# Kernel optimization log

Measured on AMD Instinct MI355X. Metric: run time of the kernel, lower is better.

## Reference

```python
import jax, jax.numpy as jnp
import numpy as np

HIDDEN = 1024
HEADS = 16
HEAD = HIDDEN // HEADS


def setup_inputs() -> dict:
    key = jax.random.key(0)
    ks = jax.random.split(key, 10)
    s = 1.0 / np.sqrt(HIDDEN)
    inp = {
        "x": jax.random.normal(ks[0], (2, 2048, HIDDEN), dtype=jnp.float32),
        "Wq": jax.random.uniform(ks[1], (HIDDEN, HIDDEN), jnp.float32, -s, s),
        "bq": jnp.zeros((HIDDEN,), jnp.float32),
        "Wk": jax.random.uniform(ks[2], (HIDDEN, HIDDEN), jnp.float32, -s, s),
        "bk": jnp.zeros((HIDDEN,), jnp.float32),
        "Wv": jax.random.uniform(ks[3], (HIDDEN, HIDDEN), jnp.float32, -s, s),
        "bv": jnp.zeros((HIDDEN,), jnp.float32),
        "Wo": jax.random.uniform(ks[4], (HIDDEN, HIDDEN), jnp.float32, -s, s),
        "bo": jnp.zeros((HIDDEN,), jnp.float32),
        "ln_g": jnp.ones((HIDDEN,), jnp.float32),
        "ln_b": jnp.zeros((HIDDEN,), jnp.float32),
    }
    return inp


def reference(x, Wq, bq, Wk, bk, Wv, bv, Wo, bo, ln_g, ln_b):
    B, S, H = x.shape
    # pre-LN (eps=1e-5 like torch LayerNorm)
    mu = jnp.mean(x, axis=-1, keepdims=True)
    var = jnp.mean(jnp.square(x - mu), axis=-1, keepdims=True)
    xn = (x - mu) * jax.lax.rsqrt(var + 1e-5) * ln_g + ln_b
    # QKV projections (torch Linear: x @ W.T + b) -> [B,S,heads,head]
    q = (xn @ Wq.T + bq).reshape(B, S, HEADS, HEAD)
    k = (xn @ Wk.T + bk).reshape(B, S, HEADS, HEAD)
    v = (xn @ Wv.T + bv).reshape(B, S, HEADS, HEAD)
    # scaled dot-product attention, naive full scores [B,heads,S,S]
    scores = jnp.einsum("bqhd,bkhd->bhqk", q, k) / jnp.sqrt(jnp.float32(HEAD))
    attn = jax.nn.softmax(scores, axis=-1)
    ctx = jnp.einsum("bhqk,bkhd->bqhd", attn, v).reshape(B, S, H)
    out = ctx @ Wo.T + bo
    return x + out  # dropout is identity in eval
```

## Files before the change

kernel.cpp:

```cpp
#include <hip/hip_runtime.h>
#include <hip/hip_bf16.h>
#include <stdint.h>

#define HID 1024
#define SEQ 2048
#define BATCH 2
#define NHEADS 16
#define HEADDIM 64
#define MROWS (BATCH*SEQ)

#define GAS __attribute__((address_space(1)))
#define LAS __attribute__((address_space(3)))

typedef __attribute__((ext_vector_type(8))) __bf16 bf16x8;
typedef __attribute__((ext_vector_type(4))) float f32x4;
typedef __attribute__((ext_vector_type(16))) float f32x16;

__device__ __forceinline__ ushort f2bf(float f) {
  union { float f; uint32_t u; } v; v.f = f;
  return (ushort)((v.u + 0x7FFFu + ((v.u >> 16) & 1u)) >> 16);
}

__device__ __forceinline__ void gl_lds16(const void* g, void* l) {
  __builtin_amdgcn_global_load_lds((const GAS void*)g, (LAS void*)l, 16, 0, 0);
}

__device__ __forceinline__ uint32_t cvtpk(float a, float b) {
  uint32_t r;
  asm("v_cvt_pk_bf16_f32 %0, %1, %2" : "=v"(r) : "v"(a), "v"(b));
  return r;
}

__device__ __forceinline__ void pl32swap(uint32_t& a, uint32_t& b) {
  asm("v_permlane32_swap_b32 %0, %1" : "+v"(a), "+v"(b));
}

__global__ __launch_bounds__(256) void k_cvt(const float* __restrict__ Wq,
                                             const float* __restrict__ Wk,
                                             const float* __restrict__ Wv,
                                             const float* __restrict__ Wo,
                                             ushort* __restrict__ dst) {
  int mat = blockIdx.y;
  const float* src = (mat == 0) ? Wq : (mat == 1) ? Wk : (mat == 2) ? Wv : Wo;
  int off = (blockIdx.x * 256 + threadIdx.x) * 4;
  float4 v = *(const float4*)(src + off);
  ushort4 o;
  o.x = f2bf(v.x); o.y = f2bf(v.y); o.z = f2bf(v.z); o.w = f2bf(v.w);
  *(ushort4*)(dst + (size_t)mat * (HID * HID) + off) = o;
}

__global__ __launch_bounds__(256) void k_ln(const float* __restrict__ x,
                                            const float* __restrict__ g,
                                            const float* __restrict__ b,
                                            ushort* __restrict__ xn) {
  int row = blockIdx.x;
  int t = threadIdx.x;
  const float* xr = x + (size_t)row * HID;
  float4 v = *(const float4*)(xr + t * 4);
  float s = v.x + v.y + v.z + v.w;
  float s2 = v.x * v.x + v.y * v.y + v.z * v.z + v.w * v.w;
  for (int m = 1; m < 64; m <<= 1) { s += __shfl_xor(s, m); s2 += __shfl_xor(s2, m); }
  __shared__ float ws[4], ws2[4];
  int wid = t >> 6;
  if ((t & 63) == 0) { ws[wid] = s; ws2[wid] = s2; }
  __syncthreads();
  s = ws[0] + ws[1] + ws[2] + ws[3];
  s2 = ws2[0] + ws2[1] + ws2[2] + ws2[3];
  float mu = s * (1.0f / HID);
  float var = s2 * (1.0f / HID) - mu * mu;
  float rstd = rsqrtf(var + 1e-5f);
  float4 gg = *(const float4*)(g + t * 4);
  float4 bb = *(const float4*)(b + t * 4);
  ushort4 o;
  o.x = f2bf((v.x - mu) * rstd * gg.x + bb.x);
  o.y = f2bf((v.y - mu) * rstd * gg.y + bb.y);
  o.z = f2bf((v.z - mu) * rstd * gg.z + bb.z);
  o.w = f2bf((v.w - mu) * rstd * gg.w + bb.w);
  *(ushort4*)(xn + (size_t)row * HID + t * 4) = o;
}

__global__ __launch_bounds__(256) void k_qkv(const ushort* __restrict__ xn,
                                             const ushort* __restrict__ wmat,
                                             const float* __restrict__ bq,
                                             const float* __restrict__ bk,
                                             const float* __restrict__ bv,
                                             ushort* __restrict__ qo,
                                             ushort* __restrict__ ko,
                                             ushort* __restrict__ vo) {
  __shared__ ushort As[128 * 32];
  __shared__ ushort Bs[128 * 32];
  int tid = threadIdx.x;
  int lane = tid & 63;
  int wv = tid >> 6;
  int quad = lane >> 4;
  int l16 = lane & 15;
  int m0 = blockIdx.x * 128;
  int ng = blockIdx.y * 128;
  int mat = ng >> 10;
  int nloc = ng & 1023;
  const ushort* wptr = wmat + (size_t)mat * (HID * HID) + (size_t)nloc * HID;
  const float* bias = (mat == 0) ? bq : (mat == 1) ? bk : bv;
  ushort* outp = (mat == 0) ? qo : (mat == 1) ? ko : vo;
  const float scl = (mat == 0) ? 0.18033688011112042f : 1.0f;

  int arow = tid >> 2;
  int acol = (tid & 3) * 8;
  int wm = (wv >> 1) * 64, wn = (wv & 1) * 64;

  f32x4 acc[4][4] = {};
  for (int k0 = 0; k0 < HID; k0 += 32) {
    __syncthreads();
    for (int t = 0; t < 2; t++) {
      gl_lds16(xn + (size_t)(m0 + t * 64 + arow) * HID + k0 + acol,
               As + t * 2048 + wv * 512);
      gl_lds16(wptr + (size_t)(t * 64 + arow) * HID + k0 + acol,
               Bs + t * 2048 + wv * 512);
    }
    __syncthreads();
    bf16x8 af[4], bfr[4];
    for (int i = 0; i < 4; i++)
      af[i] = *(const bf16x8*)&As[(wm + i * 16 + l16) * 32 + quad * 8];
    for (int n = 0; n < 4; n++)
      bfr[n] = *(const bf16x8*)&Bs[(wn + n * 16 + l16) * 32 + quad * 8];
    for (int i = 0; i < 4; i++)
      for (int n = 0; n < 4; n++)
        acc[i][n] = __builtin_amdgcn_mfma_f32_16x16x32_bf16(af[i], bfr[n], acc[i][n], 0, 0, 0);
  }
  float bv4[4];
  for (int n = 0; n < 4; n++) bv4[n] = bias[nloc + wn + n * 16 + l16];
  for (int i = 0; i < 4; i++) {
    int mrow = m0 + wm + i * 16 + quad * 4;
    for (int n = 0; n < 4; n++) {
      int col = nloc + wn + n * 16 + l16;
      int h = col >> 6, d = col & 63;
      for (int r = 0; r < 4; r++) {
        int m = mrow + r;
        int bidx = m >> 11, sidx = m & 2047;
        size_t dst;
        if (mat == 2)
          dst = (((size_t)(bidx * NHEADS + h) * HEADDIM) + d) * SEQ + sidx;
        else
          dst = (((size_t)(bidx * NHEADS + h) * SEQ) + sidx) * HEADDIM + d;
        outp[dst] = f2bf((acc[i][n][r] + bv4[n]) * scl);
      }
    }
  }
}

#define E2(x) __builtin_amdgcn_exp2f(x)

#define SOFTMAX_PF(S0, S1)                                                     \
    union { uint32_t u[4]; bf16x8 v; } pf0, pf1, pf2, pf3;                     \
    {                                                                          \
      uint32_t c0 = cvtpk(E2(S0[0]),  E2(S0[1]));                              \
      uint32_t c1 = cvtpk(E2(S0[2]),  E2(S0[3]));                              \
      uint32_t c2 = cvtpk(E2(S0[4]),  E2(S0[5]));                              \
      uint32_t c3 = cvtpk(E2(S0[6]),  E2(S0[7]));                              \
      uint32_t c4 = cvtpk(E2(S0[8]),  E2(S0[9]));                              \
      uint32_t c5 = cvtpk(E2(S0[10]), E2(S0[11]));                             \
      uint32_t c6 = cvtpk(E2(S0[12]), E2(S0[13]));                             \
      uint32_t c7 = cvtpk(E2(S0[14]), E2(S0[15]));                             \
      pl32swap(c0, c2); pl32swap(c1, c3); pl32swap(c4, c6); pl32swap(c5, c7);  \
      pf0.u[0] = c0; pf0.u[1] = c1; pf0.u[2] = c2; pf0.u[3] = c3;              \
      pf1.u[0] = c4; pf1.u[1] = c5; pf1.u[2] = c6; pf1.u[3] = c7;              \
    }                                                                          \
    {                                                                          \
      uint32_t c0 = cvtpk(E2(S1[0]),  E2(S1[1]));                              \
      uint32_t c1 = cvtpk(E2(S1[2]),  E2(S1[3]));                              \
      uint32_t c2 = cvtpk(E2(S1[4]),  E2(S1[5]));                              \
      uint32_t c3 = cvtpk(E2(S1[6]),  E2(S1[7]));                              \
      uint32_t c4 = cvtpk(E2(S1[8]),  E2(S1[9]));                              \
      uint32_t c5 = cvtpk(E2(S1[10]), E2(S1[11]));                             \
      uint32_t c6 = cvtpk(E2(S1[12]), E2(S1[13]));                             \
      uint32_t c7 = cvtpk(E2(S1[14]), E2(S1[15]));                             \
      pl32swap(c0, c2); pl32swap(c1, c3); pl32swap(c4, c6); pl32swap(c5, c7);  \
      pf2.u[0] = c0; pf2.u[1] = c1; pf2.u[2] = c2; pf2.u[3] = c3;              \
      pf3.u[0] = c4; pf3.u[1] = c5; pf3.u[2] = c6; pf3.u[3] = c7;              \
    }

#define ATTN_BODY(T, SC0, SC1, SP0, SP1, DO_DMA, WAITN)                        \
  do {                                                                         \
    if (DO_DMA) {                                                              \
      size_t ko = (size_t)((T) + 2) * 64 * HEADDIM;                            \
      size_t vo = (size_t)((T) + 2) * 64;                                      \
      gl_lds16(kSrcA + ko, &Ksm[kd][ldsA]);                                    \
      gl_lds16(kSrcB + ko, &Ksm[kd][ldsB]);                                    \
      gl_lds16(vSrcA + vo, &Vsm[vd][ldsA]);                                    \
      gl_lds16(vSrcB + vo, &Vsm[vd][ldsB]);                                    \
    }                                                                          \
    SC0 = (f32x16){}; SC1 = (f32x16){};                                        \
    __builtin_amdgcn_s_setprio(1);                                             \
    _Pragma("unroll")                                                          \
    for (int f = 0; f < 4; f++) {                                              \
      int g = 2 * f + hi;                                                      \
      bf16x8 k0 = *(const bf16x8*)&Ksm[kr][l32 * 64 + ((g ^ rsw) * 8)];        \
      bf16x8 k1 = *(const bf16x8*)&Ksm[kr][(32 + l32) * 64 + ((g ^ rsw) * 8)]; \
      SC0 = __builtin_amdgcn_mfma_f32_32x32x16_bf16(k0, qf[f], SC0, 0, 0, 0);  \
      SC1 = __builtin_amdgcn_mfma_f32_32x32x16_bf16(k1, qf[f], SC1, 0, 0, 0);  \
    }                                                                          \
    __builtin_amdgcn_s_setprio(0);                                             \
    bf16x8 vf[8];                                                              \
    _Pragma("unroll")                                                          \
    for (int kf = 0; kf < 4; kf++) {                                           \
      int g = 2 * kf + hi;                                                     \
      vf[2 * kf]     = *(const bf16x8*)&Vsm[vr][l32 * 64 + ((g ^ rsw) * 8)];   \
      vf[2 * kf + 1] = *(const bf16x8*)&Vsm[vr][(32 + l32) * 64 + ((g ^ rsw) * 8)]; \
    }                                                                          \
    SOFTMAX_PF(SP0, SP1)                                                       \
    __builtin_amdgcn_s_setprio(1);                                             \
    _Pragma("unroll")                                                          \
    for (int kf = 0; kf < 4; kf++) {                                           \
      bf16x8 pv = (kf == 0) ? pf0.v : (kf == 1) ? pf1.v : (kf == 2) ? pf2.v : pf3.v; \
      Oa0 = __builtin_amdgcn_mfma_f32_32x32x16_bf16(pv, vf[2 * kf], Oa0, 0, 0, 0);   \
      Oa1 = __builtin_amdgcn_mfma_f32_32x32x16_bf16(pv, vf[2 * kf + 1], Oa1, 0, 0, 0); \
      Os  = __builtin_amdgcn_mfma_f32_32x32x16_bf16(pv, ones, Os, 0, 0, 0);    \
    }                                                                          \
    __builtin_amdgcn_s_setprio(0);                                             \
    asm volatile("s_waitcnt vmcnt(" #WAITN ")" ::: "memory");                  \
    __builtin_amdgcn_s_barrier();                                              \
    __builtin_amdgcn_sched_barrier(0);                                         \
    kr = (kr == 2) ? 0 : kr + 1;                                               \
    kd = (kd == 2) ? 0 : kd + 1;                                               \
    vr = (vr + 1) & 3;                                                         \
    vd = (vd + 1) & 3;                                                         \
  } while (0)

__global__ __launch_bounds__(256, 2) void k_attn(const ushort* __restrict__ Q,
                                                 const ushort* __restrict__ K,
                                                 const ushort* __restrict__ Vt,
                                                 ushort* __restrict__ ctx) {
  __shared__ ushort Ksm[3][64 * 64];
  __shared__ ushort Vsm[4][64 * 64];
  int tid = threadIdx.x, lane = tid & 63, wv = tid >> 6;
  int l32 = lane & 31, hi = lane >> 5;
  int bh = blockIdx.x;
  int q0 = blockIdx.y * 128;
  const ushort* Qb = Q + ((size_t)bh * SEQ + q0 + wv * 32 + l32) * HEADDIM;
  const ushort* Kb = K + (size_t)bh * SEQ * HEADDIM;
  const ushort* Vb = Vt + (size_t)bh * HEADDIM * SEQ;

  bf16x8 qf[4];
#pragma unroll
  for (int f = 0; f < 4; f++)
    qf[f] = *(const bf16x8*)(Qb + f * 16 + hi * 8);

  bf16x8 ones;
#pragma unroll
  for (int j = 0; j < 8; j++) ones[j] = (__bf16)1.0f;

  int gsl = lane & 7;
  int rowA = wv * 8 + (lane >> 3);
  int rowB = 32 + wv * 8 + (lane >> 3);
  const ushort* kSrcA = Kb + rowA * HEADDIM + ((gsl ^ (rowA & 7)) * 8);
  const ushort* kSrcB = Kb + rowB * HEADDIM + ((gsl ^ (rowB & 7)) * 8);
  const ushort* vSrcA = Vb + (size_t)rowA * SEQ + ((gsl ^ (rowA & 7)) * 8);
  const ushort* vSrcB = Vb + (size_t)rowB * SEQ + ((gsl ^ (rowB & 7)) * 8);
  int ldsA = wv * 512;
  int ldsB = 2048 + wv * 512;

  f32x16 Oa0 = {}, Oa1 = {}, Os = {};
  f32x16 sA0, sA1, sB0, sB1;
  int rsw = (l32 & 7);

  gl_lds16(kSrcA, &Ksm[0][ldsA]);
  gl_lds16(kSrcB, &Ksm[0][ldsB]);
  gl_lds16(vSrcA, &Vsm[0][ldsA]);
  gl_lds16(vSrcB, &Vsm[0][ldsB]);
  gl_lds16(kSrcA + 64 * HEADDIM, &Ksm[1][ldsA]);
  gl_lds16(kSrcB + 64 * HEADDIM, &Ksm[1][ldsB]);
  gl_lds16(vSrcA + 64, &Vsm[1][ldsA]);
  gl_lds16(vSrcB + 64, &Vsm[1][ldsB]);
  asm volatile("s_waitcnt vmcnt(4)" ::: "memory");
  __builtin_amdgcn_s_barrier();
  __builtin_amdgcn_sched_barrier(0);

  {
    gl_lds16(kSrcA + 2 * 64 * HEADDIM, &Ksm[2][ldsA]);
    gl_lds16(kSrcB + 2 * 64 * HEADDIM, &Ksm[2][ldsB]);
    gl_lds16(vSrcA + 2 * 64, &Vsm[2][ldsA]);
    gl_lds16(vSrcB + 2 * 64, &Vsm[2][ldsB]);
    sA0 = (f32x16){}; sA1 = (f32x16){};
    __builtin_amdgcn_s_setprio(1);
#pragma unroll
    for (int f = 0; f < 4; f++) {
      int g = 2 * f + hi;
      bf16x8 k0 = *(const bf16x8*)&Ksm[0][l32 * 64 + ((g ^ rsw) * 8)];
      bf16x8 k1 = *(const bf16x8*)&Ksm[0][(32 + l32) * 64 + ((g ^ rsw) * 8)];
      sA0 = __builtin_amdgcn_mfma_f32_32x32x16_bf16(k0, qf[f], sA0, 0, 0, 0);
      sA1 = __builtin_amdgcn_mfma_f32_32x32x16_bf16(k1, qf[f], sA1, 0, 0, 0);
    }
    __builtin_amdgcn_s_setprio(0);
    asm volatile("s_waitcnt vmcnt(4)" ::: "memory");
    __builtin_amdgcn_s_barrier();
    __builtin_amdgcn_sched_barrier(0);
  }

  int kr = 1, kd = 0, vr = 0, vd = 3;
  for (int t = 1; t < 29; t += 2) {
    ATTN_BODY(t,     sB0, sB1, sA0, sA1, true, 4);
    ATTN_BODY(t + 1, sA0, sA1, sB0, sB1, true, 4);
  }
  ATTN_BODY(29, sB0, sB1, sA0, sA1, true, 4);
  ATTN_BODY(30, sA0, sA1, sB0, sB1, false, 0);

  {
    sB0 = (f32x16){}; sB1 = (f32x16){};
    __builtin_amdgcn_s_setprio(1);
#pragma unroll
    for (int f = 0; f < 4; f++) {
      int g = 2 * f + hi;
      bf16x8 k0 = *(const bf16x8*)&Ksm[kr][l32 * 64 + ((g ^ rsw) * 8)];
      bf16x8 k1 = *(const bf16x8*)&Ksm[kr][(32 + l32) * 64 + ((g ^ rsw) * 8)];
      sB0 = __builtin_amdgcn_mfma_f32_32x32x16_bf16(k0, qf[f], sB0, 0, 0, 0);
      sB1 = __builtin_amdgcn_mfma_f32_32x32x16_bf16(k1, qf[f], sB1, 0, 0, 0);
    }
    __builtin_amdgcn_s_setprio(0);
    bf16x8 vf[8];
#pragma unroll
    for (int kf = 0; kf < 4; kf++) {
      int g = 2 * kf + hi;
      vf[2 * kf]     = *(const bf16x8*)&Vsm[vr][l32 * 64 + ((g ^ rsw) * 8)];
      vf[2 * kf + 1] = *(const bf16x8*)&Vsm[vr][(32 + l32) * 64 + ((g ^ rsw) * 8)];
    }
    SOFTMAX_PF(sA0, sA1)
    __builtin_amdgcn_s_setprio(1);
#pragma unroll
    for (int kf = 0; kf < 4; kf++) {
      bf16x8 pv = (kf == 0) ? pf0.v : (kf == 1) ? pf1.v : (kf == 2) ? pf2.v : pf3.v;
      Oa0 = __builtin_amdgcn_mfma_f32_32x32x16_bf16(pv, vf[2 * kf], Oa0, 0, 0, 0);
      Oa1 = __builtin_amdgcn_mfma_f32_32x32x16_bf16(pv, vf[2 * kf + 1], Oa1, 0, 0, 0);
      Os  = __builtin_amdgcn_mfma_f32_32x32x16_bf16(pv, ones, Os, 0, 0, 0);
    }
    __builtin_amdgcn_s_setprio(0);
    vr = (vr + 1) & 3;
  }

  {
    bf16x8 vf[8];
#pragma unroll
    for (int kf = 0; kf < 4; kf++) {
      int g = 2 * kf + hi;
      vf[2 * kf]     = *(const bf16x8*)&Vsm[vr][l32 * 64 + ((g ^ rsw) * 8)];
      vf[2 * kf + 1] = *(const bf16x8*)&Vsm[vr][(32 + l32) * 64 + ((g ^ rsw) * 8)];
    }
    SOFTMAX_PF(sB0, sB1)
    __builtin_amdgcn_s_setprio(1);
#pragma unroll
    for (int kf = 0; kf < 4; kf++) {
      bf16x8 pv = (kf == 0) ? pf0.v : (kf == 1) ? pf1.v : (kf == 2) ? pf2.v : pf3.v;
      Oa0 = __builtin_amdgcn_mfma_f32_32x32x16_bf16(pv, vf[2 * kf], Oa0, 0, 0, 0);
      Oa1 = __builtin_amdgcn_mfma_f32_32x32x16_bf16(pv, vf[2 * kf + 1], Oa1, 0, 0, 0);
      Os  = __builtin_amdgcn_mfma_f32_32x32x16_bf16(pv, ones, Os, 0, 0, 0);
    }
    __builtin_amdgcn_s_setprio(0);
  }

  int bidx = bh >> 4, h = bh & 15;
#pragma unroll
  for (int r = 0; r < 16; r++) {
    float inv = 1.0f / Os[r];
    int qloc = (r & 3) + 8 * (r >> 2) + 4 * hi;
    int sidx = q0 + wv * 32 + qloc;
    size_t base = ((size_t)(bidx * SEQ) + sidx) * HID + h * HEADDIM;
    ctx[base + l32]      = f2bf(Oa0[r] * inv);
    ctx[base + 32 + l32] = f2bf(Oa1[r] * inv);
  }
}

__global__ __launch_bounds__(256) void k_oproj(const ushort* __restrict__ ctx,
                                               const ushort* __restrict__ wmat,
                                               const float* __restrict__ bo,
                                               const float* __restrict__ x,
                                               float* __restrict__ out) {
  __shared__ ushort As[128 * 32];
  __shared__ ushort Bs[128 * 32];
  int tid = threadIdx.x;
  int lane = tid & 63;
  int wv = tid >> 6;
  int quad = lane >> 4;
  int l16 = lane & 15;
  int m0 = blockIdx.x * 128;
  int n0 = blockIdx.y * 128;
  const ushort* wptr = wmat + (size_t)3 * (HID * HID) + (size_t)n0 * HID;
  int arow = tid >> 2;
  int acol = (tid & 3) * 8;
  int wm = (wv >> 1) * 64, wn = (wv & 1) * 64;

  f32x4 acc[4][4] = {};
  for (int k0 = 0; k0 < HID; k0 += 32) {
    __syncthreads();
    for (int t = 0; t < 2; t++) {
      gl_lds16(ctx + (size_t)(m0 + t * 64 + arow) * HID + k0 + acol,
               As + t * 2048 + wv * 512);
      gl_lds16(wptr + (size_t)(t * 64 + arow) * HID + k0 + acol,
               Bs + t * 2048 + wv * 512);
    }
    __syncthreads();
    bf16x8 af[4], bfr[4];
    for (int i = 0; i < 4; i++)
      af[i] = *(const bf16x8*)&As[(wm + i * 16 + l16) * 32 + quad * 8];
    for (int n = 0; n < 4; n++)
      bfr[n] = *(const bf16x8*)&Bs[(wn + n * 16 + l16) * 32 + quad * 8];
    for (int i = 0; i < 4; i++)
      for (int n = 0; n < 4; n++)
        acc[i][n] = __builtin_amdgcn_mfma_f32_16x16x32_bf16(af[i], bfr[n], acc[i][n], 0, 0, 0);
  }
  float bv4[4];
  for (int n = 0; n < 4; n++) bv4[n] = bo[n0 + wn + n * 16 + l16];
  for (int i = 0; i < 4; i++) {
    int mrow = m0 + wm + i * 16 + quad * 4;
    for (int n = 0; n < 4; n++) {
      int col = n0 + wn + n * 16 + l16;
      for (int r = 0; r < 4; r++) {
        size_t idx = (size_t)(mrow + r) * HID + col;
        out[idx] = acc[i][n][r] + bv4[n] + x[idx];
      }
    }
  }
}

extern "C" void kernel_launch(void* const* d_in, const int* in_sizes, int n_in,
                              void* d_out, int out_size, void* d_ws, size_t ws_size,
                              hipStream_t stream) {
  const float* x    = (const float*)d_in[0];
  const float* Wq   = (const float*)d_in[1];
  const float* bq   = (const float*)d_in[2];
  const float* Wk   = (const float*)d_in[3];
  const float* bk   = (const float*)d_in[4];
  const float* Wv   = (const float*)d_in[5];
  const float* bv   = (const float*)d_in[6];
  const float* Wo   = (const float*)d_in[7];
  const float* bo   = (const float*)d_in[8];
  const float* ln_g = (const float*)d_in[9];
  const float* ln_b = (const float*)d_in[10];
  float* out = (float*)d_out;

  const size_t MB = 1024 * 1024;
  ushort* ws_w = (ushort*)d_ws;
  ushort* xn   = (ushort*)((char*)d_ws + 8 * MB);
  ushort* Qw   = (ushort*)((char*)d_ws + 16 * MB);
  ushort* Kw   = (ushort*)((char*)d_ws + 24 * MB);
  ushort* Vw   = (ushort*)((char*)d_ws + 32 * MB);
  ushort* Cw   = (ushort*)((char*)d_ws + 40 * MB);

  k_cvt<<<dim3(1024, 4), 256, 0, stream>>>(Wq, Wk, Wv, Wo, ws_w);
  k_ln<<<dim3(MROWS), 256, 0, stream>>>(x, ln_g, ln_b, xn);
  k_qkv<<<dim3(32, 24), 256, 0, stream>>>(xn, ws_w, bq, bk, bv, Qw, Kw, Vw);
  k_attn<<<dim3(BATCH * NHEADS, SEQ / 128), 256, 0, stream>>>(Qw, Kw, Vw, Cw);
  k_oproj<<<dim3(32, 8), 256, 0, stream>>>(Cw, ws_w, bo, x, out);
}
```

Measured before the change: 200.4 us.

## Split attention key tiles across wave pairs with LDS cross-wave reduction

Reorganizes the attention kernel so each wave handles 64 query rows and half of each 64-key tile, instead of 32 query rows and the full tile. Each K fragment read from LDS is now reused for two Q fragments, which halves per-wave LDS reads of K and V. The two key-halves' partial outputs and row sums are combined at the end through an LDS reduction in a reused arena. The cost is more accumulator registers per wave, extra barriers, and a final reduction step.

```diff
diff --git a/kernel.cpp b/kernel.cpp
--- a/kernel.cpp
+++ b/kernel.cpp
@@ -148,6 +148,7 @@
 }
 
 #define E2(x) __builtin_amdgcn_exp2f(x)
+#define MFMA(a, b, c) __builtin_amdgcn_mfma_f32_32x32x16_bf16(a, b, c, 0, 0, 0)
 
 #define SOFTMAX_PF(S0, S1)                                                     \
     union { uint32_t u[4]; bf16x8 v; } pf0, pf1, pf2, pf3;                     \
@@ -178,71 +179,72 @@
       pf3.u[0] = c4; pf3.u[1] = c5; pf3.u[2] = c6; pf3.u[3] = c7;              \
     }
 
+#define PV_STEP(VS, SP0, SP1)                                                  \
+    bf16x8 vf00 = *(const bf16x8*)&VSM(VS)[l32 * 64 + (((wk4 + hi) ^ rsw) * 8)];           \
+    bf16x8 vf10 = *(const bf16x8*)&VSM(VS)[l32 * 64 + (((wk4 + 2 + hi) ^ rsw) * 8)];       \
+    bf16x8 vf01 = *(const bf16x8*)&VSM(VS)[(32 + l32) * 64 + (((wk4 + hi) ^ rsw) * 8)];    \
+    bf16x8 vf11 = *(const bf16x8*)&VSM(VS)[(32 + l32) * 64 + (((wk4 + 2 + hi) ^ rsw) * 8)];\
+    SOFTMAX_PF(SP0, SP1)                                                       \
+    __builtin_amdgcn_s_setprio(1);                                             \
+    Oa00 = MFMA(pf0.v, vf00, Oa00); Oa00 = MFMA(pf1.v, vf10, Oa00);            \
+    Oa01 = MFMA(pf0.v, vf01, Oa01); Oa01 = MFMA(pf1.v, vf11, Oa01);            \
+    Oa10 = MFMA(pf2.v, vf00, Oa10); Oa10 = MFMA(pf3.v, vf10, Oa10);            \
+    Oa11 = MFMA(pf2.v, vf01, Oa11); Oa11 = MFMA(pf3.v, vf11, Oa11);            \
+    Os0  = MFMA(pf0.v, ones, Os0);  Os0  = MFMA(pf1.v, ones, Os0);             \
+    Os1  = MFMA(pf2.v, ones, Os1);  Os1  = MFMA(pf3.v, ones, Os1);             \
+    __builtin_amdgcn_s_setprio(0);
+
 #define ATTN_BODY(T, SC0, SC1, SP0, SP1, DO_DMA, WAITN)                        \
   do {                                                                         \
     if (DO_DMA) {                                                              \
       size_t ko = (size_t)((T) + 2) * 64 * HEADDIM;                            \
       size_t vo = (size_t)((T) + 2) * 64;                                      \
-      gl_lds16(kSrcA + ko, &Ksm[kd][ldsA]);                                    \
-      gl_lds16(kSrcB + ko, &Ksm[kd][ldsB]);                                    \
-      gl_lds16(vSrcA + vo, &Vsm[vd][ldsA]);                                    \
-      gl_lds16(vSrcB + vo, &Vsm[vd][ldsB]);                                    \
+      gl_lds16(kSrcA + ko, KSM(kd) + ldsA);                                    \
+      gl_lds16(kSrcB + ko, KSM(kd) + ldsB);                                    \
+      gl_lds16(vSrcA + vo, VSM(vd) + ldsA);                                    \
+      gl_lds16(vSrcB + vo, VSM(vd) + ldsB);                                    \
     }                                                                          \
     SC0 = (f32x16){}; SC1 = (f32x16){};                                        \
     __builtin_amdgcn_s_setprio(1);                                             \
     _Pragma("unroll")                                                          \
     for (int f = 0; f < 4; f++) {                                              \
-      int g = 2 * f + hi;                                                      \
-      bf16x8 k0 = *(const bf16x8*)&Ksm[kr][l32 * 64 + ((g ^ rsw) * 8)];        \
-      bf16x8 k1 = *(const bf16x8*)&Ksm[kr][(32 + l32) * 64 + ((g ^ rsw) * 8)]; \
-      SC0 = __builtin_amdgcn_mfma_f32_32x32x16_bf16(k0, qf[f], SC0, 0, 0, 0);  \
-      SC1 = __builtin_amdgcn_mfma_f32_32x32x16_bf16(k1, qf[f], SC1, 0, 0, 0);  \
+      bf16x8 kfr = *(const bf16x8*)&KSM(kr)[(wk32 + l32) * 64 +                \
+                                            (((2 * f + hi) ^ rsw) * 8)];       \
+      SC0 = MFMA(kfr, qf0[f], SC0);                                            \
+      SC1 = MFMA(kfr, qf1[f], SC1);                                            \
     }                                                                          \
     __builtin_amdgcn_s_setprio(0);                                             \
-    bf16x8 vf[8];                                                              \
-    _Pragma("unroll")                                                          \
-    for (int kf = 0; kf < 4; kf++) {                                           \
-      int g = 2 * kf + hi;                                                     \
-      vf[2 * kf]     = *(const bf16x8*)&Vsm[vr][l32 * 64 + ((g ^ rsw) * 8)];   \
-      vf[2 * kf + 1] = *(const bf16x8*)&Vsm[vr][(32 + l32) * 64 + ((g ^ rsw) * 8)]; \
-    }                                                                          \
-    SOFTMAX_PF(SP0, SP1)                                                       \
-    __builtin_amdgcn_s_setprio(1);                                             \
-    _Pragma("unroll")                                                          \
-    for (int kf = 0; kf < 4; kf++) {                                           \
-      bf16x8 pv = (kf == 0) ? pf0.v : (kf == 1) ? pf1.v : (kf == 2) ? pf2.v : pf3.v; \
-      Oa0 = __builtin_amdgcn_mfma_f32_32x32x16_bf16(pv, vf[2 * kf], Oa0, 0, 0, 0);   \
-      Oa1 = __builtin_amdgcn_mfma_f32_32x32x16_bf16(pv, vf[2 * kf + 1], Oa1, 0, 0, 0); \
-      Os  = __builtin_amdgcn_mfma_f32_32x32x16_bf16(pv, ones, Os, 0, 0, 0);    \
-    }                                                                          \
-    __builtin_amdgcn_s_setprio(0);                                             \
+    PV_STEP(vr, SP0, SP1)                                                      \
     asm volatile("s_waitcnt vmcnt(" #WAITN ")" ::: "memory");                  \
     __builtin_amdgcn_s_barrier();                                              \
     __builtin_amdgcn_sched_barrier(0);                                         \
-    kr = (kr == 2) ? 0 : kr + 1;                                               \
-    kd = (kd == 2) ? 0 : kd + 1;                                               \
-    vr = (vr + 1) & 3;                                                         \
-    vd = (vd + 1) & 3;                                                         \
+    kr = (kr == 2) ? 0 : kr + 1;  kd = (kd == 2) ? 0 : kd + 1;                 \
+    vr = (vr + 1) & 3;  vd = (vd + 1) & 3;                                     \
   } while (0)
 
 __global__ __launch_bounds__(256, 2) void k_attn(const ushort* __restrict__ Q,
                                                  const ushort* __restrict__ K,
                                                  const ushort* __restrict__ Vt,
                                                  ushort* __restrict__ ctx) {
-  __shared__ ushort Ksm[3][64 * 64];
-  __shared__ ushort Vsm[4][64 * 64];
+  __shared__ __align__(16) unsigned char arena[57344];
+#define KSM(i) ((ushort*)arena + (i) * 4096)
+#define VSM(i) ((ushort*)(arena + 24576) + (i) * 4096)
   int tid = threadIdx.x, lane = tid & 63, wv = tid >> 6;
   int l32 = lane & 31, hi = lane >> 5;
+  int wq = wv & 1, wk = wv >> 1;
+  int wk32 = wk * 32, wk4 = wk * 4;
   int bh = blockIdx.x;
   int q0 = blockIdx.y * 128;
-  const ushort* Qb = Q + ((size_t)bh * SEQ + q0 + wv * 32 + l32) * HEADDIM;
+  const ushort* Qb = Q + ((size_t)bh * SEQ + q0 + wq * 64 + l32) * HEADDIM;
   const ushort* Kb = K + (size_t)bh * SEQ * HEADDIM;
   const ushort* Vb = Vt + (size_t)bh * HEADDIM * SEQ;
 
-  bf16x8 qf[4];
+  bf16x8 qf0[4], qf1[4];
 #pragma unroll
-  for (int f = 0; f < 4; f++)
-    qf[f] = *(const bf16x8*)(Qb + f * 16 + hi * 8);
+  for (int f = 0; f < 4; f++) {
+    qf0[f] = *(const bf16x8*)(Qb + f * 16 + hi * 8);
+    qf1[f] = *(const bf16x8*)(Qb + 32 * HEADDIM + f * 16 + hi * 8);
+  }
 
   bf16x8 ones;
 #pragma unroll
@@ -258,36 +260,34 @@
   int ldsA = wv * 512;
   int ldsB = 2048 + wv * 512;
 
-  f32x16 Oa0 = {}, Oa1 = {}, Os = {};
+  f32x16 Oa00 = {}, Oa01 = {}, Oa10 = {}, Oa11 = {}, Os0 = {}, Os1 = {};
   f32x16 sA0, sA1, sB0, sB1;
   int rsw = (l32 & 7);
 
-  gl_lds16(kSrcA, &Ksm[0][ldsA]);
-  gl_lds16(kSrcB, &Ksm[0][ldsB]);
-  gl_lds16(vSrcA, &Vsm[0][ldsA]);
-  gl_lds16(vSrcB, &Vsm[0][ldsB]);
-  gl_lds16(kSrcA + 64 * HEADDIM, &Ksm[1][ldsA]);
-  gl_lds16(kSrcB + 64 * HEADDIM, &Ksm[1][ldsB]);
-  gl_lds16(vSrcA + 64, &Vsm[1][ldsA]);
-  gl_lds16(vSrcB + 64, &Vsm[1][ldsB]);
+  gl_lds16(kSrcA, KSM(0) + ldsA);
+  gl_lds16(kSrcB, KSM(0) + ldsB);
+  gl_lds16(vSrcA, VSM(0) + ldsA);
+  gl_lds16(vSrcB, VSM(0) + ldsB);
+  gl_lds16(kSrcA + 64 * HEADDIM, KSM(1) + ldsA);
+  gl_lds16(kSrcB + 64 * HEADDIM, KSM(1) + ldsB);
+  gl_lds16(vSrcA + 64, VSM(1) + ldsA);
+  gl_lds16(vSrcB + 64, VSM(1) + ldsB);
   asm volatile("s_waitcnt vmcnt(4)" ::: "memory");
   __builtin_amdgcn_s_barrier();
   __builtin_amdgcn_sched_barrier(0);
 
   {
-    gl_lds16(kSrcA + 2 * 64 * HEADDIM, &Ksm[2][ldsA]);
-    gl_lds16(kSrcB + 2 * 64 * HEADDIM, &Ksm[2][ldsB]);
-    gl_lds16(vSrcA + 2 * 64, &Vsm[2][ldsA]);
-    gl_lds16(vSrcB + 2 * 64, &Vsm[2][ldsB]);
+    gl_lds16(kSrcA + 2 * 64 * HEADDIM, KSM(2) + ldsA);
+    gl_lds16(kSrcB + 2 * 64 * HEADDIM, KSM(2) + ldsB);
+    gl_lds16(vSrcA + 2 * 64, VSM(2) + ldsA);
+    gl_lds16(vSrcB + 2 * 64, VSM(2) + ldsB);
     sA0 = (f32x16){}; sA1 = (f32x16){};
     __builtin_amdgcn_s_setprio(1);
 #pragma unroll
     for (int f = 0; f < 4; f++) {
-      int g = 2 * f + hi;
-      bf16x8 k0 = *(const bf16x8*)&Ksm[0][l32 * 64 + ((g ^ rsw) * 8)];
-      bf16x8 k1 = *(const bf16x8*)&Ksm[0][(32 + l32) * 64 + ((g ^ rsw) * 8)];
-      sA0 = __builtin_amdgcn_mfma_f32_32x32x16_bf16(k0, qf[f], sA0, 0, 0, 0);
-      sA1 = __builtin_amdgcn_mfma_f32_32x32x16_bf16(k1, qf[f], sA1, 0, 0, 0);
+      bf16x8 kfr = *(const bf16x8*)&KSM(0)[(wk32 + l32) * 64 + (((2 * f + hi) ^ rsw) * 8)];
+      sA0 = MFMA(kfr, qf0[f], sA0);
+      sA1 = MFMA(kfr, qf1[f], sA1);
     }
     __builtin_amdgcn_s_setprio(0);
     asm volatile("s_waitcnt vmcnt(4)" ::: "memory");
@@ -308,63 +308,65 @@
     __builtin_amdgcn_s_setprio(1);
 #pragma unroll
     for (int f = 0; f < 4; f++) {
-      int g = 2 * f + hi;
-      bf16x8 k0 = *(const bf16x8*)&Ksm[kr][l32 * 64 + ((g ^ rsw) * 8)];
-      bf16x8 k1 = *(const bf16x8*)&Ksm[kr][(32 + l32) * 64 + ((g ^ rsw) * 8)];
-      sB0 = __builtin_amdgcn_mfma_f32_32x32x16_bf16(k0, qf[f], sB0, 0, 0, 0);
-      sB1 = __builtin_amdgcn_mfma_f32_32x32x16_bf16(k1, qf[f], sB1, 0, 0, 0);
+      bf16x8 kfr = *(const bf16x8*)&KSM(kr)[(wk32 + l32) * 64 + (((2 * f + hi) ^ rsw) * 8)];
+      sB0 = MFMA(kfr, qf0[f], sB0);
+      sB1 = MFMA(kfr, qf1[f], sB1);
     }
     __builtin_amdgcn_s_setprio(0);
-    bf16x8 vf[8];
+    PV_STEP(vr, sA0, sA1)
+    vr = (vr + 1) & 3;
+  }
+  {
+    PV_STEP(vr, sB0, sB1)
+  }
+
+  __builtin_amdgcn_s_barrier();
+  float* red = (float*)arena;
+  int rbase = wq * 6144;
+#define WR4(T, VEC, C)                                                         \
+  *(f32x4*)&red[rbase + ((T) * 4 + (C)) * 256 + lane * 4] =                    \
+      (f32x4){(VEC)[(C)*4+0], (VEC)[(C)*4+1], (VEC)[(C)*4+2], (VEC)[(C)*4+3]};
+#define WR16(T, VEC) WR4(T, VEC, 0) WR4(T, VEC, 1) WR4(T, VEC, 2) WR4(T, VEC, 3)
+#define RD4(T, VEC, C) {                                                       \
+  f32x4 t_ = *(const f32x4*)&red[rbase + ((T) * 4 + (C)) * 256 + lane * 4];    \
+  (VEC)[(C)*4+0] += t_[0]; (VEC)[(C)*4+1] += t_[1];                            \
+  (VEC)[(C)*4+2] += t_[2]; (VEC)[(C)*4+3] += t_[3]; }
+#define RD16(T, VEC) RD4(T, VEC, 0) RD4(T, VEC, 1) RD4(T, VEC, 2) RD4(T, VEC, 3)
+  if (wk == 1) {
+    WR16(0, Oa00) WR16(1, Oa01) WR16(2, Oa10) WR16(3, Oa11)
+    WR16(4, Os0)  WR16(5, Os1)
+  }
+  asm volatile("s_waitcnt lgkmcnt(0)" ::: "memory");
+  __builtin_amdgcn_s_barrier();
+  if (wk == 0) {
+    RD16(0, Oa00) RD16(1, Oa01) RD16(2, Oa10) RD16(3, Oa11)
+    RD16(4, Os0)  RD16(5, Os1)
+    int bidx = bh >> 4, h = bh & 15;
 #pragma unroll
-    for (int kf = 0; kf < 4; kf++) {
-      int g = 2 * kf + hi;
-      vf[2 * kf]     = *(const bf16x8*)&Vsm[vr][l32 * 64 + ((g ^ rsw) * 8)];
-      vf[2 * kf + 1] = *(const bf16x8*)&Vsm[vr][(32 + l32) * 64 + ((g ^ rsw) * 8)];
-    }
-    SOFTMAX_PF(sA0, sA1)
-    __builtin_amdgcn_s_setprio(1);
-#pragma unroll
-    for (int kf = 0; kf < 4; kf++) {
-      bf16x8 pv = (kf == 0) ? pf0.v : (kf == 1) ? pf1.v : (kf == 2) ? pf2.v : pf3.v;
-      Oa0 = __builtin_amdgcn_mfma_f32_32x32x16_bf16(pv, vf[2 * kf], Oa0, 0, 0, 0);
-      Oa1 = __builtin_amdgcn_mfma_f32_32x32x16_bf16(pv, vf[2 * kf + 1], Oa1, 0, 0, 0);
-      Os  = __builtin_amdgcn_mfma_f32_32x32x16_bf16(pv, ones, Os, 0, 0, 0);
-    }
-    __builtin_amdgcn_s_setprio(0);
-    vr = (vr + 1) & 3;
-  }
-
-  {
-    bf16x8 vf[8];
-#pragma unroll
-    for (int kf = 0; kf < 4; kf++) {
-      int g = 2 * kf + hi;
-      vf[2 * kf]     = *(const bf16x8*)&Vsm[vr][l32 * 64 + ((g ^ rsw) * 8)];
-      vf[2 * kf + 1] = *(const bf16x8*)&Vsm[vr][(32 + l32) * 64 + ((g ^ rsw) * 8)];
-    }
-    SOFTMAX_PF(sB0, sB1)
-    __builtin_amdgcn_s_setprio(1);
-#pragma unroll
-    for (int kf = 0; kf < 4; kf++) {
-      bf16x8 pv = (kf == 0) ? pf0.v : (kf == 1) ? pf1.v : (kf == 2) ? pf2.v : pf3.v;
-      Oa0 = __builtin_amdgcn_mfma_f32_32x32x16_bf16(pv, vf[2 * kf], Oa0, 0, 0, 0);
-      Oa1 = __builtin_amdgcn_mfma_f32_32x32x16_bf16(pv, vf[2 * kf + 1], Oa1, 0, 0, 0);
-      Os  = __builtin_amdgcn_mfma_f32_32x32x16_bf16(pv, ones, Os, 0, 0, 0);
-    }
-    __builtin_amdgcn_s_setprio(0);
-  }
-
-  int bidx = bh >> 4, h = bh & 15;
-#pragma unroll
-  for (int r = 0; r < 16; r++) {
-    float inv = 1.0f / Os[r];
-    int qloc = (r & 3) + 8 * (r >> 2) + 4 * hi;
-    int sidx = q0 + wv * 32 + qloc;
-    size_t base = ((size_t)(bidx * SEQ) + sidx) * HID + h * HEADDIM;
-    ctx[base + l32]      = f2bf(Oa0[r] * inv);
-    ctx[base + 32 + l32] = f2bf(Oa1[r] * inv);
-  }
+    for (int r = 0; r < 16; r++) {
+      int crow = (r & 3) + 8 * (r >> 2) + 4 * hi;
+      {
+        float inv = 1.0f / Os0[r];
+        int sidx = q0 + wq * 64 + crow;
+        size_t b2 = ((size_t)(bidx * SEQ) + sidx) * HID + h * HEADDIM;
+        ctx[b2 + l32]      = f2bf(Oa00[r] * inv);
+        ctx[b2 + 32 + l32] = f2bf(Oa01[r] * inv);
+      }
+      {
+        float inv = 1.0f / Os1[r];
+        int sidx = q0 + wq * 64 + 32 + crow;
+        size_t b2 = ((size_t)(bidx * SEQ) + sidx) * HID + h * HEADDIM;
+        ctx[b2 + l32]      = f2bf(Oa10[r] * inv);
+        ctx[b2 + 32 + l32] = f2bf(Oa11[r] * inv);
+      }
+    }
+  }
+#undef KSM
+#undef VSM
+#undef WR4
+#undef WR16
+#undef RD4
+#undef RD16
 }
 
 __global__ __launch_bounds__(256) void k_oproj(const ushort* __restrict__ ctx,
```

Result: slower. 204.8 us (+2.2%).

## Triple-buffer LDS tiles in QKV and output-projection GEMMs with async prefetch

Applied to the files above, without the earlier changes.

Replaces the single-buffered load-sync-compute loop in the QKV and output projection GEMMs with a three-stage LDS ring. Global-to-LDS loads for the tile two steps ahead are issued while MFMAs run on the current tile, using explicit vmcnt waits and one barrier per iteration instead of two. It also raises wave priority around the MFMA block. The goal is to hide global memory latency behind compute, at the cost of three times the LDS per block, which may reduce occupancy.

```diff
diff --git a/kernel.cpp b/kernel.cpp
--- a/kernel.cpp
+++ b/kernel.cpp
@@ -79,6 +79,14 @@
   *(ushort4*)(xn + (size_t)row * HID + t * 4) = o;
 }
 
+#define GSTAGE(KOFF, B)                                                        \
+  do {                                                                         \
+    gl_lds16(a0 + (KOFF), &As[B][wv * 512]);                                   \
+    gl_lds16(a1 + (KOFF), &As[B][2048 + wv * 512]);                            \
+    gl_lds16(b0 + (KOFF), &Bs[B][wv * 512]);                                   \
+    gl_lds16(b1 + (KOFF), &Bs[B][2048 + wv * 512]);                            \
+  } while (0)
+
 __global__ __launch_bounds__(256) void k_qkv(const ushort* __restrict__ xn,
                                              const ushort* __restrict__ wmat,
                                              const float* __restrict__ bq,
@@ -87,8 +95,8 @@
                                              ushort* __restrict__ qo,
                                              ushort* __restrict__ ko,
                                              ushort* __restrict__ vo) {
-  __shared__ ushort As[128 * 32];
-  __shared__ ushort Bs[128 * 32];
+  __shared__ ushort As[3][128 * 32];
+  __shared__ ushort Bs[3][128 * 32];
   int tid = threadIdx.x;
   int lane = tid & 63;
   int wv = tid >> 6;
@@ -107,25 +115,48 @@
   int acol = (tid & 3) * 8;
   int wm = (wv >> 1) * 64, wn = (wv & 1) * 64;
 
+  const ushort* a0 = xn + (size_t)(m0 + arow) * HID + acol;
+  const ushort* a1 = xn + (size_t)(m0 + 64 + arow) * HID + acol;
+  const ushort* b0 = wptr + (size_t)arow * HID + acol;
+  const ushort* b1 = wptr + (size_t)(64 + arow) * HID + acol;
+
   f32x4 acc[4][4] = {};
-  for (int k0 = 0; k0 < HID; k0 += 32) {
-    __syncthreads();
-    for (int t = 0; t < 2; t++) {
-      gl_lds16(xn + (size_t)(m0 + t * 64 + arow) * HID + k0 + acol,
-               As + t * 2048 + wv * 512);
-      gl_lds16(wptr + (size_t)(t * 64 + arow) * HID + k0 + acol,
-               Bs + t * 2048 + wv * 512);
-    }
-    __syncthreads();
+
+  GSTAGE(0, 0);
+  GSTAGE(32, 1);
+  asm volatile("s_waitcnt vmcnt(4)" ::: "memory");
+  __builtin_amdgcn_s_barrier();
+  __builtin_amdgcn_sched_barrier(0);
+
+  int cr = 0, dw = 2;
+  for (int kk = 0; kk < 32; kk++) {
+    if (kk < 30) GSTAGE((kk + 2) * 32, dw);
     bf16x8 af[4], bfr[4];
+#pragma unroll
     for (int i = 0; i < 4; i++)
-      af[i] = *(const bf16x8*)&As[(wm + i * 16 + l16) * 32 + quad * 8];
+      af[i] = *(const bf16x8*)&As[cr][(wm + i * 16 + l16) * 32 + quad * 8];
+#pragma unroll
     for (int n = 0; n < 4; n++)
-      bfr[n] = *(const bf16x8*)&Bs[(wn + n * 16 + l16) * 32 + quad * 8];
+      bfr[n] = *(const bf16x8*)&Bs[cr][(wn + n * 16 + l16) * 32 + quad * 8];
+    __builtin_amdgcn_s_setprio(1);
+#pragma unroll
     for (int i = 0; i < 4; i++)
+#pragma unroll
       for (int n = 0; n < 4; n++)
         acc[i][n] = __builtin_amdgcn_mfma_f32_16x16x32_bf16(af[i], bfr[n], acc[i][n], 0, 0, 0);
-  }
+    __builtin_amdgcn_s_setprio(0);
+    if (kk < 30)
+      asm volatile("s_waitcnt vmcnt(4)" ::: "memory");
+    else if (kk == 30)
+      asm volatile("s_waitcnt vmcnt(0)" ::: "memory");
+    if (kk < 31) {
+      __builtin_amdgcn_s_barrier();
+      __builtin_amdgcn_sched_barrier(0);
+    }
+    cr = (cr == 2) ? 0 : cr + 1;
+    dw = (dw == 2) ? 0 : dw + 1;
+  }
+
   float bv4[4];
   for (int n = 0; n < 4; n++) bv4[n] = bias[nloc + wn + n * 16 + l16];
   for (int i = 0; i < 4; i++) {
@@ -372,8 +403,8 @@
                                                const float* __restrict__ bo,
                                                const float* __restrict__ x,
                                                float* __restrict__ out) {
-  __shared__ ushort As[128 * 32];
-  __shared__ ushort Bs[128 * 32];
+  __shared__ ushort As[3][128 * 32];
+  __shared__ ushort Bs[3][128 * 32];
   int tid = threadIdx.x;
   int lane = tid & 63;
   int wv = tid >> 6;
@@ -386,25 +417,48 @@
   int acol = (tid & 3) * 8;
   int wm = (wv >> 1) * 64, wn = (wv & 1) * 64;
 
+  const ushort* a0 = ctx + (size_t)(m0 + arow) * HID + acol;
+  const ushort* a1 = ctx + (size_t)(m0 + 64 + arow) * HID + acol;
+  const ushort* b0 = wptr + (size_t)arow * HID + acol;
+  const ushort* b1 = wptr + (size_t)(64 + arow) * HID + acol;
+
   f32x4 acc[4][4] = {};
-  for (int k0 = 0; k0 < HID; k0 += 32) {
-    __syncthreads();
-    for (int t = 0; t < 2; t++) {
-      gl_lds16(ctx + (size_t)(m0 + t * 64 + arow) * HID + k0 + acol,
-               As + t * 2048 + wv * 512);
-      gl_lds16(wptr + (size_t)(t * 64 + arow) * HID + k0 + acol,
-               Bs + t * 2048 + wv * 512);
-    }
-    __syncthreads();
+
+  GSTAGE(0, 0);
+  GSTAGE(32, 1);
+  asm volatile("s_waitcnt vmcnt(4)" ::: "memory");
+  __builtin_amdgcn_s_barrier();
+  __builtin_amdgcn_sched_barrier(0);
+
+  int cr = 0, dw = 2;
+  for (int kk = 0; kk < 32; kk++) {
+    if (kk < 30) GSTAGE((kk + 2) * 32, dw);
     bf16x8 af[4], bfr[4];
+#pragma unroll
     for (int i = 0; i < 4; i++)
-      af[i] = *(const bf16x8*)&As[(wm + i * 16 + l16) * 32 + quad * 8];
+      af[i] = *(const bf16x8*)&As[cr][(wm + i * 16 + l16) * 32 + quad * 8];
+#pragma unroll
     for (int n = 0; n < 4; n++)
-      bfr[n] = *(const bf16x8*)&Bs[(wn + n * 16 + l16) * 32 + quad * 8];
+      bfr[n] = *(const bf16x8*)&Bs[cr][(wn + n * 16 + l16) * 32 + quad * 8];
+    __builtin_amdgcn_s_setprio(1);
+#pragma unroll
     for (int i = 0; i < 4; i++)
+#pragma unroll
       for (int n = 0; n < 4; n++)
         acc[i][n] = __builtin_amdgcn_mfma_f32_16x16x32_bf16(af[i], bfr[n], acc[i][n], 0, 0, 0);
-  }
+    __builtin_amdgcn_s_setprio(0);
+    if (kk < 30)
+      asm volatile("s_waitcnt vmcnt(4)" ::: "memory");
+    else if (kk == 30)
+      asm volatile("s_waitcnt vmcnt(0)" ::: "memory");
+    if (kk < 31) {
+      __builtin_amdgcn_s_barrier();
+      __builtin_amdgcn_sched_barrier(0);
+    }
+    cr = (cr == 2) ? 0 : cr + 1;
+    dw = (dw == 2) ? 0 : dw + 1;
+  }
+
   float bv4[4];
   for (int n = 0; n < 4; n++) bv4[n] = bo[n0 + wn + n * 16 + l16];
   for (int i = 0; i < 4; i++) {
```

Result: slower. 206.9 us (+3.2%).
